# Kernel optimization log

Measured on AMD Instinct MI355X. Metric: run time of the kernel, lower is better.

Reference implementation:

```python
import jax, jax.numpy as jnp
import numpy as np

B, D, NH, HH, WW = 16, 384, 12, 48, 48
MLP = 4 * D


def _dwconv(x_blc, w, b, H, W):
    # depthwise 3x3 conv on (B,L,C) token map laid out as HxW
    Bsz, L, C = x_blc.shape
    xn = x_blc.reshape(Bsz, H, W, C).transpose(0, 3, 1, 2)  # NCHW
    y = jax.lax.conv_general_dilated(
        xn, w, (1, 1), 'SAME', feature_group_count=C,
        dimension_numbers=('NCHW', 'OIHW', 'NCHW'))
    y = y + b[None, :, None, None]
    return y.transpose(0, 2, 3, 1).reshape(Bsz, L, C)


def _ln(x, w, b):
    m = jnp.mean(x, -1, keepdims=True)
    v = jnp.mean(jnp.square(x - m), -1, keepdims=True)
    return (x - m) * jax.lax.rsqrt(v + 1e-5) * w + b


def _rope_tables(H, W, C):
    k_max = C // 4  # feature_dim // (2 * len((h, w)))
    theta = 1.0 / (10000.0 ** (jnp.arange(k_max, dtype=jnp.float32) / k_max))
    ah = jnp.broadcast_to((jnp.arange(H, dtype=jnp.float32)[:, None] * theta)[:, None, :], (H, W, k_max))
    aw = jnp.broadcast_to((jnp.arange(W, dtype=jnp.float32)[:, None] * theta)[None, :, :], (H, W, k_max))
    ang = jnp.concatenate([ah, aw], -1)  # (H, W, C//2)
    return jnp.cos(ang), jnp.sin(ang)


def _rope(x, cos, sin):
    # x: (B,H,W,C); complex rotation on consecutive pairs of the last dim
    xr = x.reshape(*x.shape[:-1], -1, 2)
    a, b2 = xr[..., 0], xr[..., 1]
    out = jnp.stack([cos * a - sin * b2, sin * a + cos * b2], -1)
    return out.reshape(x.shape)


def _forward(x, H, W, cpe1_w, cpe1_b, norm1_w, norm1_b, in_proj_w, in_proj_b,
             act_proj_w, act_proj_b, dwc_w, dwc_b, qk_w, qk_b, lepe_w, lepe_b,
             out_proj_w, out_proj_b, cpe2_w, cpe2_b, norm2_w, norm2_b,
             fc1_w, fc1_b, fc2_w, fc2_b):
    Bsz, L, C = x.shape
    nh = NH
    hd = C // nh

    x = x + _dwconv(x, cpe1_w, cpe1_b, H, W)
    shortcut = x
    xn = _ln(x, norm1_w, norm1_b)
    act_res = jax.nn.silu(xn @ act_proj_w.T + act_proj_b)
    xi = xn @ in_proj_w.T + in_proj_b
    xi = jax.nn.silu(_dwconv(xi, dwc_w, dwc_b, H, W))

    # --- linear (kernelized) attention with RoPE ---
    qk = xi @ qk_w.T + qk_b  # (B, L, 2C)
    q = jax.nn.elu(qk[..., :C]) + 1.0
    k = jax.nn.elu(qk[..., C:]) + 1.0
    cos, sin = _rope_tables(H, W, C)
    q_rope = _rope(q.reshape(Bsz, H, W, C), cos, sin).reshape(Bsz, L, nh, hd).transpose(0, 2, 1, 3)
    k_rope = _rope(k.reshape(Bsz, H, W, C), cos, sin).reshape(Bsz, L, nh, hd).transpose(0, 2, 1, 3)
    qh = q.reshape(Bsz, L, nh, hd).transpose(0, 2, 1, 3)
    kh = k.reshape(Bsz, L, nh, hd).transpose(0, 2, 1, 3)
    vh = xi.reshape(Bsz, L, nh, hd).transpose(0, 2, 1, 3)

    z = 1.0 / (jnp.einsum('bhnd,bhd->bhn', qh, kh.mean(axis=2)) + 1e-6)  # (B,nh,L)
    kv = jnp.einsum('bhnd,bhne->bhde', k_rope, vh) / L                   # (B,nh,hd,hd)
    att = jnp.einsum('bhnd,bhde->bhne', q_rope, kv) * z[..., None]
    att = att.transpose(0, 2, 1, 3).reshape(Bsz, L, C)
    att = att + _dwconv(xi, lepe_w, lepe_b, H, W)  # lepe on v (== xi)

    out = (att * act_res) @ out_proj_w.T + out_proj_b
    x = shortcut + out
    x = x + _dwconv(x, cpe2_w, cpe2_b, H, W)
    xn2 = _ln(x, norm2_w, norm2_b)
    h1 = jax.nn.gelu(xn2 @ fc1_w.T + fc1_b, approximate=False)
    x = x + (h1 @ fc2_w.T + fc2_b)
    return x


def setup_inputs() -> dict:
    key = jax.random.key(0)
    ks = jax.random.split(key, 16)
    def w(k, shape, s=0.02):
        return jax.random.normal(k, shape, jnp.float32) * s
    return {
        'x': jax.random.normal(ks[0], (B, HH * WW, D), jnp.float32),
        'H': HH, 'W': WW,
        'cpe1_w': w(ks[1], (D, 1, 3, 3)), 'cpe1_b': jnp.zeros((D,), jnp.float32),
        'norm1_w': jnp.ones((D,), jnp.float32), 'norm1_b': jnp.zeros((D,), jnp.float32),
        'in_proj_w': w(ks[2], (D, D)), 'in_proj_b': jnp.zeros((D,), jnp.float32),
        'act_proj_w': w(ks[3], (D, D)), 'act_proj_b': jnp.zeros((D,), jnp.float32),
        'dwc_w': w(ks[4], (D, 1, 3, 3)), 'dwc_b': jnp.zeros((D,), jnp.float32),
        'qk_w': w(ks[5], (2 * D, D)), 'qk_b': jnp.zeros((2 * D,), jnp.float32),
        'lepe_w': w(ks[6], (D, 1, 3, 3)), 'lepe_b': jnp.zeros((D,), jnp.float32),
        'out_proj_w': w(ks[7], (D, D)), 'out_proj_b': jnp.zeros((D,), jnp.float32),
        'cpe2_w': w(ks[8], (D, 1, 3, 3)), 'cpe2_b': jnp.zeros((D,), jnp.float32),
        'norm2_w': jnp.ones((D,), jnp.float32), 'norm2_b': jnp.zeros((D,), jnp.float32),
        'fc1_w': w(ks[9], (MLP, D)), 'fc1_b': jnp.zeros((MLP,), jnp.float32),
        'fc2_w': w(ks[10], (D, MLP)), 'fc2_b': jnp.zeros((D,), jnp.float32),
    }


def reference(x, H, W, cpe1_w, cpe1_b, norm1_w, norm1_b, in_proj_w, in_proj_b,
              act_proj_w, act_proj_b, dwc_w, dwc_b, qk_w, qk_b, lepe_w, lepe_b,
              out_proj_w, out_proj_b, cpe2_w, cpe2_b, norm2_w, norm2_b,
              fc1_w, fc1_b, fc2_w, fc2_b):
    return _forward(x, H, W, cpe1_w, cpe1_b, norm1_w, norm1_b, in_proj_w, in_proj_b,
                    act_proj_w, act_proj_b, dwc_w, dwc_b, qk_w, qk_b, lepe_w, lepe_b,
                    out_proj_w, out_proj_b, cpe2_w, cpe2_b, norm2_w, norm2_b,
                    fc1_w, fc1_b, fc2_w, fc2_b)
```

## Files before the change

### kernel.cpp

```cpp
#include <hip/hip_runtime.h>
#include <hip/hip_bf16.h>
#include <math.h>


#define L_TOK 2304
#define DIM   384
#define NHEADS 12
#define BATCH 16
#define HIMG  48
#define WIMG  48
#define UNITB ((size_t)L_TOK * DIM)

typedef unsigned short u16;
typedef __attribute__((ext_vector_type(8))) short bf16x8;
typedef __attribute__((ext_vector_type(8))) unsigned short u16x8;
typedef __attribute__((ext_vector_type(4))) float f32x4;

enum { M_BIAS = 0, M_SILU = 1, M_ELU1 = 2, M_GELU = 3, M_RES = 4 };

__device__ __forceinline__ float siluf(float x) { return x / (1.0f + __expf(-x)); }
__device__ __forceinline__ float geluf(float x) {
    float t = x * fmaf(x * x, 0.0713548162726f, 1.59576912161f);
    return x / (1.0f + __expf(-t));
}
__device__ __forceinline__ u16 f2bf(float f) {
    union { __hip_bfloat16 h; u16 u; } c;
    c.h = __float2bfloat16(f);
    return c.u;
}
__device__ __forceinline__ float bf2f(u16 u) { return __uint_as_float(((unsigned)u) << 16); }
__device__ __forceinline__ float4 bf2f4(ushort4 v) {
    return (float4){bf2f(v.x), bf2f(v.y), bf2f(v.z), bf2f(v.w)};
}
__device__ __forceinline__ void vmwait(int n) {
    if (n == 0)       asm volatile("s_waitcnt vmcnt(0)" ::: "memory");
    else if (n == 4)  asm volatile("s_waitcnt vmcnt(4)" ::: "memory");
    else if (n == 8)  asm volatile("s_waitcnt vmcnt(8)" ::: "memory");
    else if (n == 12) asm volatile("s_waitcnt vmcnt(12)" ::: "memory");
    else              asm volatile("s_waitcnt vmcnt(0)" ::: "memory");
}

__global__ void sentinel_k(float* out, float v) { out[0] = v; }

__global__ __launch_bounds__(256) void cvtw_k(const float* __restrict__ src, u16* __restrict__ dst) {
    int i = blockIdx.x * 256 + threadIdx.x;
    float4 v = ((const float4*)src)[i];
    ushort4 o;
    o.x = f2bf(v.x); o.y = f2bf(v.y); o.z = f2bf(v.z); o.w = f2bf(v.w);
    ((ushort4*)dst)[i] = o;
}

__global__ __launch_bounds__(256) void rope_tab_k(float* __restrict__ cosT, float* __restrict__ sinT) {
    int i = blockIdx.x * 256 + threadIdx.x;
    if (i >= L_TOK * 192) return;
    int n = i / 192, p = i % 192;
    int h = n / WIMG, w = n % WIMG;
    int j = (p < 96) ? p : p - 96;
    float pos = (p < 96) ? (float)h : (float)w;
    float theta = expf(-(float)j * (9.210340371976184f / 96.0f));
    float ang = pos * theta;
    cosT[i] = cosf(ang);
    sinT[i] = sinf(ang);
}

#define FMA4(s, a, ww) { s.x = fmaf(a.x, ww.x, s.x); s.y = fmaf(a.y, ww.y, s.y); \
                         s.z = fmaf(a.z, ww.z, s.z); s.w = fmaf(a.w, ww.w, s.w); }

__global__ __launch_bounds__(256) void dwconvf_k(const float* __restrict__ src,
                                                 const float* __restrict__ wgt,
                                                 const float* __restrict__ bias,
                                                 float* __restrict__ outf) {
    const int col = blockIdx.x * 256 + threadIdx.x;
    const int strip = blockIdx.y & 3;
    const int b = blockIdx.y >> 2;
    const int cg = col % 96, w = col / 96;
    const int rs = WIMG * DIM;
    const size_t ibase = (size_t)b * UNITB + (size_t)w * DIM + cg * 4;
    const float* srcb = src + ibase;
    const float4 z4 = {0.f, 0.f, 0.f, 0.f};
    float4 w9[9];
#pragma unroll
    for (int t = 0; t < 9; ++t) {
        const int c = cg * 4;
        w9[t] = (float4){wgt[(c + 0) * 9 + t], wgt[(c + 1) * 9 + t],
                         wgt[(c + 2) * 9 + t], wgt[(c + 3) * 9 + t]};
    }
    const float4 bv = ((const float4*)bias)[cg];
    float4 A0, A1, A2, B0, B1, B2, C0, C1, C2;
    auto ldrow = [&](int hh, float4& L0, float4& L1, float4& L2) {
        if ((unsigned)hh >= (unsigned)HIMG) { L0 = z4; L1 = z4; L2 = z4; return; }
        const float* p = srcb + (size_t)hh * rs;
        L0 = (w > 0)        ? *(const float4*)(p - DIM) : z4;
        L1 = *(const float4*)p;
        L2 = (w < WIMG - 1) ? *(const float4*)(p + DIM) : z4;
    };
    const int h0 = strip * 12;
    ldrow(h0 - 1, A0, A1, A2);
    ldrow(h0,     B0, B1, B2);
    for (int h = h0; h < h0 + 12; ++h) {
        ldrow(h + 1, C0, C1, C2);
        float4 s = bv;
        FMA4(s, A0, w9[0]); FMA4(s, A1, w9[1]); FMA4(s, A2, w9[2]);
        FMA4(s, B0, w9[3]); FMA4(s, B1, w9[4]); FMA4(s, B2, w9[5]);
        FMA4(s, C0, w9[6]); FMA4(s, C1, w9[7]); FMA4(s, C2, w9[8]);
        const size_t idx = ibase + (size_t)h * rs;
        s.x += B1.x; s.y += B1.y; s.z += B1.z; s.w += B1.w;
        *(float4*)(outf + idx) = s;
        A0 = B0; A1 = B1; A2 = B2;
        B0 = C0; B1 = C1; B2 = C2;
    }
}

__global__ __launch_bounds__(256) void dwconvb_k(const u16* __restrict__ src,
                                                 const float* __restrict__ wgt,
                                                 const float* __restrict__ bias,
                                                 const u16* __restrict__ att,
                                                 const u16* __restrict__ act,
                                                 u16* __restrict__ outb, int mode) {
    const int col = blockIdx.x * 256 + threadIdx.x;
    const int strip = blockIdx.y & 3;
    const int b = blockIdx.y >> 2;
    const int cg = col % 96, w = col / 96;
    const int rs = WIMG * DIM;
    const size_t ibase = (size_t)b * UNITB + (size_t)w * DIM + cg * 4;
    const u16* srcb = src + ibase;
    const float4 z4 = {0.f, 0.f, 0.f, 0.f};
    float4 w9[9];
#pragma unroll
    for (int t = 0; t < 9; ++t) {
        const int c = cg * 4;
        w9[t] = (float4){wgt[(c + 0) * 9 + t], wgt[(c + 1) * 9 + t],
                         wgt[(c + 2) * 9 + t], wgt[(c + 3) * 9 + t]};
    }
    const float4 bv = ((const float4*)bias)[cg];
    float4 A0, A1, A2, B0, B1, B2, C0, C1, C2;
    auto ldrow = [&](int hh, float4& L0, float4& L1, float4& L2) {
        if ((unsigned)hh >= (unsigned)HIMG) { L0 = z4; L1 = z4; L2 = z4; return; }
        const u16* p = srcb + (size_t)hh * rs;
        L0 = (w > 0)        ? bf2f4(*(const ushort4*)(p - DIM)) : z4;
        L1 = bf2f4(*(const ushort4*)p);
        L2 = (w < WIMG - 1) ? bf2f4(*(const ushort4*)(p + DIM)) : z4;
    };
    const int h0 = strip * 12;
    ldrow(h0 - 1, A0, A1, A2);
    ldrow(h0,     B0, B1, B2);
    for (int h = h0; h < h0 + 12; ++h) {
        ldrow(h + 1, C0, C1, C2);
        float4 s = bv;
        FMA4(s, A0, w9[0]); FMA4(s, A1, w9[1]); FMA4(s, A2, w9[2]);
        FMA4(s, B0, w9[3]); FMA4(s, B1, w9[4]); FMA4(s, B2, w9[5]);
        FMA4(s, C0, w9[6]); FMA4(s, C1, w9[7]); FMA4(s, C2, w9[8]);
        const size_t idx = ibase + (size_t)h * rs;
        ushort4 ob;
        if (mode == 1) {
            ob = (ushort4){f2bf(siluf(s.x)), f2bf(siluf(s.y)), f2bf(siluf(s.z)), f2bf(siluf(s.w))};
        } else {
            float4 a4 = bf2f4(*(const ushort4*)(att + idx));
            float4 m4 = bf2f4(*(const ushort4*)(act + idx));
            ob = (ushort4){f2bf((a4.x + s.x) * m4.x), f2bf((a4.y + s.y) * m4.y),
                           f2bf((a4.z + s.z) * m4.z), f2bf((a4.w + s.w) * m4.w)};
        }
        *(ushort4*)(outb + idx) = ob;
        A0 = B0; A1 = B1; A2 = B2;
        B0 = C0; B1 = C1; B2 = C2;
    }
}

__global__ __launch_bounds__(256) void ln_k(const float* __restrict__ in,
                                            const float* __restrict__ w,
                                            const float* __restrict__ b,
                                            u16* __restrict__ out) {
    const int row = blockIdx.x * 4 + (threadIdx.x >> 6);
    const int lane = threadIdx.x & 63;
    const float* x = in + (size_t)row * DIM;
    float v[6];
    float s = 0.f;
#pragma unroll
    for (int i = 0; i < 6; ++i) { v[i] = x[lane + i * 64]; s += v[i]; }
#pragma unroll
    for (int o = 32; o > 0; o >>= 1) s += __shfl_xor(s, o, 64);
    const float mean = s * (1.0f / DIM);
    float q = 0.f;
#pragma unroll
    for (int i = 0; i < 6; ++i) { float d = v[i] - mean; q = fmaf(d, d, q); }
#pragma unroll
    for (int o = 32; o > 0; o >>= 1) q += __shfl_xor(q, o, 64);
    const float rs = 1.0f / sqrtf(q * (1.0f / DIM) + 1e-5f);
    u16* o2 = out + (size_t)row * DIM;
#pragma unroll
    for (int i = 0; i < 6; ++i) {
        int d = lane + i * 64;
        o2[d] = f2bf(fmaf((v[i] - mean) * rs, w[d], b[d]));
    }
}

#define CHK 64
template<int K>
__global__ __launch_bounds__(256, 4) void gemm_sk(const u16* __restrict__ A, int lda,
                                                  const u16* __restrict__ Wt, int ldw,
                                                  const float* __restrict__ bias,
                                                  const float* __restrict__ bias2,
                                                  const float* __restrict__ res,
                                                  float* __restrict__ Cf, u16* __restrict__ Cb,
                                                  u16* __restrict__ Cb2,
                                                  int ldc, int mode, int mode2) {
    constexpr int NT = K / 32;
    constexpr int NCH = K / CHK;
    __shared__ u16 smem[16384];
    u16* const Bbuf[2] = {smem, smem + 8192};
    const int tid = threadIdx.x;
    const int l = tid & 63;
    const int w = tid >> 6;
    const int fr = l & 15, kb = l >> 4;
    const int T = gridDim.x * gridDim.y;
    const int d = blockIdx.y * gridDim.x + blockIdx.x;
    int flat = d;
    if ((T & 7) == 0) { const int q8 = T >> 3; flat = (d & 7) * q8 + (d >> 3); }
    const int n0 = (flat % gridDim.x) * 128;
    const int m0 = (flat / gridDim.x) * 128;
    const int sw = (fr & 7) << 4;

    f32x4 acc[2][8];
#pragma unroll
    for (int i = 0; i < 2; ++i)
#pragma unroll
        for (int j = 0; j < 8; ++j) acc[i][j] = (f32x4){0.f, 0.f, 0.f, 0.f};

    const u16* Ar0 = A + (size_t)(m0 + w * 32 + fr) * lda + kb * 8;
    const u16* Ar1 = Ar0 + (size_t)16 * lda;

    auto STAGE = [&](u16* buf, int cc) {
        const int ck0 = cc * CHK;
#pragma unroll
        for (int q = 0; q < 4; ++q) {
            const int c16 = q * 256 + tid;
            const int col = c16 >> 3;
            const int kb16 = c16 & 7;
            const int koff = ((kb16 * 16) ^ ((col & 7) << 4)) >> 1;
            const u16* g = Wt + (size_t)(n0 + col) * ldw + ck0 + koff;
            __builtin_amdgcn_global_load_lds(
                (const __attribute__((address_space(1))) void*)g,
                (__attribute__((address_space(3))) void*)(buf + (size_t)(q * 256 + w * 64) * 8),
                16, 0, 0);
        }
    };

    bf16x8 pA[4][2];
    STAGE(Bbuf[0], 0);
    __builtin_amdgcn_sched_barrier(0);
#pragma unroll
    for (int i = 0; i < 4; ++i) {
        pA[i][0] = *(const bf16x8*)(Ar0 + i * 32);
        pA[i][1] = *(const bf16x8*)(Ar1 + i * 32);
    }
    __builtin_amdgcn_sched_barrier(0);
    STAGE(Bbuf[1], 1);
    __builtin_amdgcn_sched_barrier(0);
    vmwait(12);
    __builtin_amdgcn_s_barrier();

#pragma unroll
    for (int c = 0; c < NCH; ++c) {
        const u16* bp = Bbuf[c & 1];
#pragma unroll
        for (int ks = 0; ks < 2; ++ks) {
            const int t = 2 * c + ks;
            bf16x8 a0 = pA[t & 3][0], a1 = pA[t & 3][1];
            if (t + 4 < NT) {
                pA[t & 3][0] = *(const bf16x8*)(Ar0 + (t + 4) * 32);
                pA[t & 3][1] = *(const bf16x8*)(Ar1 + (t + 4) * 32);
            }
            const int kpart = (ks * 64 + kb * 16) ^ sw;
            const char* bsb = (const char*)bp + fr * 128 + kpart;
#pragma unroll
            for (int ni = 0; ni < 8; ++ni) {
                bf16x8 bfrag = *(const bf16x8*)(bsb + ni * (16 * 128));
                acc[0][ni] = __builtin_amdgcn_mfma_f32_16x16x32_bf16(a0, bfrag, acc[0][ni], 0, 0, 0);
                acc[1][ni] = __builtin_amdgcn_mfma_f32_16x16x32_bf16(a1, bfrag, acc[1][ni], 0, 0, 0);
            }
        }
        __builtin_amdgcn_sched_barrier(0);
        __builtin_amdgcn_s_barrier();
        __builtin_amdgcn_sched_barrier(0);
        if (c + 2 < NCH) STAGE(Bbuf[c & 1], c + 2);
        __builtin_amdgcn_sched_barrier(0);
        if (c + 1 < NCH)
            vmwait((c < NCH - 2) ? 8 : 0);
    }

    const int orow = (l >> 4) * 4, ocol = l & 15;
    if (Cb != nullptr) {
        const bool is2 = (Cb2 != nullptr) && (n0 >= DIM);
        u16* dst = is2 ? Cb2 : Cb;
        const int ldcs = is2 ? DIM : ldc;
        const int nc0 = is2 ? (n0 - DIM) : n0;
        const float* bp2 = is2 ? bias2 : bias;
        const int md = is2 ? mode2 : mode;
#pragma unroll
        for (int mi = 0; mi < 2; ++mi)
#pragma unroll
            for (int ni = 0; ni < 8; ++ni) {
                const int colL = ni * 16 + ocol;
                const float bv = bp2[nc0 + colL];
#pragma unroll
                for (int r = 0; r < 4; ++r) {
                    const int rowL = w * 32 + mi * 16 + orow + r;
                    float v = acc[mi][ni][r] + bv;
                    if (md == M_SILU)      v = siluf(v);
                    else if (md == M_ELU1) v = (v > 0.f) ? (v + 1.f) : __expf(v);
                    else if (md == M_GELU) v = geluf(v);
                    smem[rowL * 128 + (colL ^ ((rowL & 7) << 3))] = f2bf(v);
                }
            }
        __builtin_amdgcn_s_barrier();
        const int rr = tid >> 4, cc = tid & 15;
#pragma unroll
        for (int it = 0; it < 8; ++it) {
            const int row = it * 16 + rr;
            u16x8 v = *(const u16x8*)&smem[row * 128 + ((cc * 8) ^ ((row & 7) << 3))];
            *(u16x8*)(dst + (size_t)(m0 + row) * ldcs + nc0 + cc * 8) = v;
        }
    } else {
        float* smf = (float*)smem;
#pragma unroll
        for (int p = 0; p < 2; ++p) {
            if (p) __builtin_amdgcn_s_barrier();
#pragma unroll
            for (int mi = 0; mi < 2; ++mi)
#pragma unroll
                for (int ni = 0; ni < 4; ++ni) {
                    const int colL = ni * 16 + ocol;
                    const float bv = bias[n0 + p * 64 + colL];
#pragma unroll
                    for (int r = 0; r < 4; ++r) {
                        const int rowL = w * 32 + mi * 16 + orow + r;
                        float v = acc[mi][p * 4 + ni][r] + bv;
                        if (mode == M_SILU)      v = siluf(v);
                        else if (mode == M_ELU1) v = (v > 0.f) ? (v + 1.f) : __expf(v);
                        else if (mode == M_GELU) v = geluf(v);
                        smf[rowL * 64 + (colL ^ ((rowL & 3) << 4))] = v;
                    }
                }
            __builtin_amdgcn_s_barrier();
            const int rr = tid >> 4, cc = tid & 15;
#pragma unroll
            for (int it = 0; it < 8; ++it) {
                const int row = it * 16 + rr;
                float4 v = *(const float4*)&smf[row * 64 + ((cc * 4) ^ ((row & 3) << 4))];
                const size_t oi = (size_t)(m0 + row) * ldc + n0 + p * 64 + cc * 4;
                if (res) {
                    float4 rv = *(const float4*)(res + oi);
                    v.x += rv.x; v.y += rv.y; v.z += rv.z; v.w += rv.w;
                }
                *(float4*)(Cf + oi) = v;
            }
        }
    }
}

__global__ __launch_bounds__(384) void kmean_part_k(const u16* __restrict__ kbuf, float* __restrict__ part, int nb) {
    const int b = blockIdx.x, chunk = blockIdx.y;
    const int c = threadIdx.x;
    const u16* p = kbuf + ((size_t)(b * L_TOK + chunk * 256)) * DIM + c;
    float s = 0.f;
    for (int n = 0; n < 256; ++n) s += bf2f(p[(size_t)n * DIM]);
    part[(size_t)(chunk * nb + b) * DIM + c] = s;
}

__global__ __launch_bounds__(384) void kmean_fin_k(const float* __restrict__ part, float* __restrict__ km, int nb) {
    const int b = blockIdx.x, c = threadIdx.x;
    float s = 0.f;
#pragma unroll
    for (int ch = 0; ch < 9; ++ch) s += part[(size_t)(ch * nb + b) * DIM + c];
    km[b * DIM + c] = s * (1.0f / L_TOK);
}

__global__ __launch_bounds__(256) void kv_part_k(const u16* __restrict__ kbuf, const u16* __restrict__ xi,
                                                 const float* __restrict__ cosT, const float* __restrict__ sinT,
                                                 float* __restrict__ part) {
    const int bh = blockIdx.x >> 2, chunk = blockIdx.x & 3;
    const int b = bh / NHEADS, h = bh % NHEADS;
    __shared__ float ks[64][33];
    __shared__ float vs[64][33];
    const int tid = threadIdx.x;
    const int e0 = (tid & 15) * 2;
    const int d0 = (tid >> 4) * 2;
    float acc00 = 0.f, acc01 = 0.f, acc10 = 0.f, acc11 = 0.f;
    const int nbeg = chunk * 576, nend = nbeg + 576;
    for (int n0 = nbeg; n0 < nend; n0 += 64) {
#pragma unroll
        for (int j = 0; j < 4; ++j) {
            int pi = tid + j * 256;
            int tn = pi >> 4;
            int pd = pi & 15;
            int n = n0 + tn;
            unsigned kk = *(const unsigned*)(kbuf + ((size_t)(b * L_TOK + n)) * DIM + h * 32 + pd * 2);
            float ka = bf2f((u16)(kk & 0xffffu)), kb2 = bf2f((u16)(kk >> 16));
            float cs = cosT[n * 192 + h * 16 + pd];
            float sn = sinT[n * 192 + h * 16 + pd];
            ks[tn][pd * 2]     = cs * ka - sn * kb2;
            ks[tn][pd * 2 + 1] = sn * ka + cs * kb2;
        }
#pragma unroll
        for (int j = 0; j < 4; ++j) {
            int pi = tid + j * 256;
            int tn = pi >> 4;
            int dd = (pi & 15) * 2;
            unsigned vv = *(const unsigned*)(xi + ((size_t)(b * L_TOK + n0 + tn)) * DIM + h * 32 + dd);
            vs[tn][dd]     = bf2f((u16)(vv & 0xffffu));
            vs[tn][dd + 1] = bf2f((u16)(vv >> 16));
        }
        __syncthreads();
#pragma unroll 8
        for (int n = 0; n < 64; ++n) {
            float k0v = ks[n][d0], k1v = ks[n][d0 + 1];
            float v0 = vs[n][e0], v1 = vs[n][e0 + 1];
            acc00 = fmaf(k0v, v0, acc00);
            acc01 = fmaf(k0v, v1, acc01);
            acc10 = fmaf(k1v, v0, acc10);
            acc11 = fmaf(k1v, v1, acc11);
        }
        __syncthreads();
    }
    float* o = part + ((size_t)blockIdx.x * 32 + d0) * 32 + e0;
    o[0] = acc00; o[1] = acc01;
    o[32] = acc10; o[33] = acc11;
}

__global__ __launch_bounds__(256) void kv_fin_k(const float* __restrict__ part, float* __restrict__ kv) {
    const int bh = blockIdx.x;
    const int tid = threadIdx.x;
#pragma unroll
    for (int i = tid; i < 1024; i += 256) {
        float s = 0.f;
#pragma unroll
        for (int c = 0; c < 4; ++c) s += part[((size_t)(bh * 4 + c)) * 1024 + i];
        kv[(size_t)bh * 1024 + i] = s * (1.0f / L_TOK);
    }
}

__global__ __launch_bounds__(384) void att_k(const u16* __restrict__ q, const float* __restrict__ kv,
                                             const float* __restrict__ km,
                                             const float* __restrict__ cosT, const float* __restrict__ sinT,
                                             u16* __restrict__ out) {
    __shared__ float kvs[NHEADS * 32 * 32];
    __shared__ float kms[DIM];
    __shared__ float sq[DIM];
    __shared__ float sqr[DIM];
    const int b = blockIdx.x / 48;
    const int chunk = blockIdx.x % 48;
    const int tid = threadIdx.x;
    for (int i = tid; i < NHEADS * 1024; i += 384) kvs[i] = kv[(size_t)b * (NHEADS * 1024) + i];
    kms[tid] = km[b * DIM + tid];
    __syncthreads();
    const int h = tid >> 5, e = tid & 31;
    const int p = tid >> 1;
    const float* kvh = &kvs[h * 1024];
    for (int ni = 0; ni < 48; ++ni) {
        const int n = chunk * 48 + ni;
        const float qv = bf2f(q[((size_t)(b * L_TOK + n)) * DIM + tid]);
        sq[tid] = qv;
        __syncthreads();
        float a = sq[tid & ~1], bb = sq[tid | 1];
        float cs = cosT[n * 192 + p], sn = sinT[n * 192 + p];
        sqr[tid] = (tid & 1) ? fmaf(sn, a, cs * bb) : fmaf(cs, a, -sn * bb);
        float zp = qv * kms[tid];
#pragma unroll
        for (int o = 16; o > 0; o >>= 1) zp += __shfl_xor(zp, o, 32);
        const float z = 1.0f / (zp + 1e-6f);
        __syncthreads();
        float dot = 0.f;
        const float* qrh = &sqr[h * 32];
#pragma unroll 8
        for (int dd = 0; dd < 32; ++dd) dot = fmaf(qrh[dd], kvh[dd * 32 + e], dot);
        out[((size_t)(b * L_TOK + n)) * DIM + tid] = f2bf(z * dot);
        __syncthreads();
    }
}

extern "C" void kernel_launch(void* const* d_in, const int* in_sizes, int n_in,
                              void* d_out, int out_size, void* d_ws, size_t ws_size,
                              hipStream_t stream) {
    const float* x       = (const float*)d_in[0];
    const float* cpe1_w  = (const float*)d_in[3];
    const float* cpe1_b  = (const float*)d_in[4];
    const float* norm1_w = (const float*)d_in[5];
    const float* norm1_b = (const float*)d_in[6];
    const float* in_w    = (const float*)d_in[7];
    const float* in_b    = (const float*)d_in[8];
    const float* act_w   = (const float*)d_in[9];
    const float* act_b   = (const float*)d_in[10];
    const float* dwc_w   = (const float*)d_in[11];
    const float* dwc_b   = (const float*)d_in[12];
    const float* qk_w    = (const float*)d_in[13];
    const float* qk_b    = (const float*)d_in[14];
    const float* lepe_w  = (const float*)d_in[15];
    const float* lepe_b  = (const float*)d_in[16];
    const float* outp_w  = (const float*)d_in[17];
    const float* outp_b  = (const float*)d_in[18];
    const float* cpe2_w  = (const float*)d_in[19];
    const float* cpe2_b  = (const float*)d_in[20];
    const float* norm2_w = (const float*)d_in[21];
    const float* norm2_b = (const float*)d_in[22];
    const float* fc1_w   = (const float*)d_in[23];
    const float* fc1_b   = (const float*)d_in[24];
    const float* fc2_w   = (const float*)d_in[25];
    const float* fc2_b   = (const float*)d_in[26];
    float* out = (float*)d_out;

    float* ws = (float*)d_ws;
    const size_t TAB = (size_t)L_TOK * 192;
    const size_t NW_IN = 147456, NW_QK = 294912, NW_FC = 589824;
    const size_t WBF_U16 = NW_IN * 3 + NW_QK + NW_FC * 2;
    const size_t KVP = 4 * (size_t)BATCH * NHEADS * 1024;
    const size_t SMALL = 2 * TAB + (size_t)BATCH * DIM + 9 * (size_t)BATCH * DIM
                       + (size_t)BATCH * NHEADS * 1024 + KVP + WBF_U16 / 2;
    float* cosT = ws;
    float* sinT = cosT + TAB;
    float* km   = sinT + TAB;
    float* part = km + (size_t)BATCH * DIM;
    float* kvb  = part + 9 * (size_t)BATCH * DIM;
    float* kvp  = kvb + (size_t)BATCH * NHEADS * 1024;
    u16*   wb_in  = (u16*)(kvp + KVP);
    u16*   wb_act = wb_in + NW_IN;
    u16*   wb_qk  = wb_act + NW_IN;
    u16*   wb_out = wb_qk + NW_QK;
    u16*   wb_fc1 = wb_out + NW_IN;
    u16*   wb_fc2 = wb_fc1 + NW_FC;
    float* gbuf = ws + SMALL;

    const size_t avail = (ws_size / 4 > SMALL) ? (ws_size / 4 - SMALL) : 0;
    int nb = 0;
    for (int cand = BATCH; cand >= 1; cand >>= 1)
        if (9 * (size_t)cand * UNITB / 2 <= avail) { nb = cand; break; }
    if (nb == 0) {
        sentinel_k<<<1, 1, 0, stream>>>(out, (float)(ws_size >> 20));
        return;
    }

    cvtw_k<<<(int)(NW_IN / 1024), 256, 0, stream>>>(in_w, wb_in);
    cvtw_k<<<(int)(NW_IN / 1024), 256, 0, stream>>>(act_w, wb_act);
    cvtw_k<<<(int)(NW_QK / 1024), 256, 0, stream>>>(qk_w, wb_qk);
    cvtw_k<<<(int)(NW_IN / 1024), 256, 0, stream>>>(outp_w, wb_out);
    cvtw_k<<<(int)(NW_FC / 1024), 256, 0, stream>>>(fc1_w, wb_fc1);
    cvtw_k<<<(int)(NW_FC / 1024), 256, 0, stream>>>(fc2_w, wb_fc2);
    rope_tab_k<<<(int)((TAB + 255) / 256), 256, 0, stream>>>(cosT, sinT);

    for (int b0 = 0; b0 < BATCH; b0 += nb) {
        const size_t goff = (size_t)b0 * UNITB;
        const size_t GU   = (size_t)nb * UNITB;
        float* W0 = gbuf;
        float* W1 = gbuf + GU;
        float* W2 = gbuf + 2 * GU;
        u16*   Wb = (u16*)(gbuf + 4 * GU);
        float* O  = out + goff;
        const float* Xg = x + goff;
        u16* xi0p = (u16*)W2;
        u16* actp = (u16*)W2 + GU;

        const dim3 DWG(18, nb * 4);
        const dim3 G384(3, nb * 18), G768(6, nb * 18), G1536(12, nb * 18);

        dwconvf_k<<<DWG, 256, 0, stream>>>(Xg, cpe1_w, cpe1_b, W0);
        ln_k<<<nb * 576, 256, 0, stream>>>(W0, norm1_w, norm1_b, (u16*)W1);
        gemm_sk<384><<<G768, 256, 0, stream>>>((u16*)W1, DIM, wb_in, DIM, in_b, act_b, nullptr,
                                               nullptr, xi0p, actp, DIM, M_BIAS, M_SILU);
        dwconvb_k<<<DWG, 256, 0, stream>>>(xi0p, dwc_w, dwc_b, nullptr, nullptr, Wb, 1);
        gemm_sk<384><<<G768, 256, 0, stream>>>(Wb, DIM, wb_qk, DIM, qk_b, qk_b + DIM, nullptr,
                                               nullptr, (u16*)W1, (u16*)O, DIM, M_ELU1, M_ELU1);
        kmean_part_k<<<dim3(nb, 9), 384, 0, stream>>>((u16*)O, part, nb);
        kmean_fin_k<<<nb, 384, 0, stream>>>(part, km, nb);
        kv_part_k<<<nb * NHEADS * 4, 256, 0, stream>>>((u16*)O, Wb, cosT, sinT, kvp);
        kv_fin_k<<<nb * NHEADS, 256, 0, stream>>>(kvp, kvb);
        att_k<<<nb * 48, 384, 0, stream>>>((u16*)W1, kvb, km, cosT, sinT, (u16*)O);
        dwconvb_k<<<DWG, 256, 0, stream>>>(Wb, lepe_w, lepe_b, (const u16*)O, actp,
                                           (u16*)W1, 3);
        gemm_sk<384><<<G384, 256, 0, stream>>>((u16*)W1, DIM, wb_out, DIM, outp_b, nullptr, W0,
                                               W2, nullptr, nullptr, DIM, M_RES, M_RES);
        dwconvf_k<<<DWG, 256, 0, stream>>>(W2, cpe2_w, cpe2_b, W0);
        ln_k<<<nb * 576, 256, 0, stream>>>(W0, norm2_w, norm2_b, (u16*)W1);
        gemm_sk<384><<<G1536, 256, 0, stream>>>((u16*)W1, DIM, wb_fc1, DIM, fc1_b, nullptr, nullptr,
                                                nullptr, (u16*)W2, nullptr, 1536, M_GELU, M_GELU);
        gemm_sk<1536><<<G384, 256, 0, stream>>>((u16*)W2, 1536, wb_fc2, 1536, fc2_b, nullptr, W0,
                                                O, nullptr, nullptr, DIM, M_RES, M_RES);
    }
}
```

Before: 611.9 us.

## Replace scalar attention apply kernel with MFMA tile kernel plus separate normalizer pass

The per-token scalar attention kernel, which used shared-memory dot products and three barriers per token, is replaced by an MFMA-based kernel. It computes RoPE(q)·kv per (batch, head, 128-row tile) using bf16 16x16x32 MFMA, with kv transposed and stored as bf16. The normalizer z = 1/(q·kmean) moves into a separate small kernel that writes a per-row buffer. This trades a per-token serialized loop for matrix-core throughput, at the cost of an extra launch, an extra buffer, and bf16 rounding of kv and rotated q.

After: 530.5 us. 1.15x faster.

```diff
diff --git a/kernel.cpp b/kernel.cpp
--- a/kernel.cpp
+++ b/kernel.cpp
@@ -375,6 +375,21 @@
     km[b * DIM + c] = s * (1.0f / L_TOK);
 }
 
+__global__ __launch_bounds__(256) void z_k(const u16* __restrict__ q, const float* __restrict__ km,
+                                           float* __restrict__ z) {
+    const int row = blockIdx.x * 4 + (threadIdx.x >> 6);
+    const int lane = threadIdx.x & 63;
+    const int b = row / L_TOK;
+    const u16* qr = q + (size_t)row * DIM;
+    const float* kb = km + b * DIM;
+    float s = 0.f;
+#pragma unroll
+    for (int i = 0; i < 6; ++i) { int c = lane + i * 64; s += bf2f(qr[c]) * kb[c]; }
+#pragma unroll
+    for (int o = 32; o > 0; o >>= 1) s += __shfl_xor(s, o, 64);
+    if (lane == 0) z[row] = 1.0f / (s + 1e-6f);
+}
+
 __global__ __launch_bounds__(256) void kv_part_k(const u16* __restrict__ kbuf, const u16* __restrict__ xi,
                                                  const float* __restrict__ cosT, const float* __restrict__ sinT,
                                                  float* __restrict__ part) {
@@ -427,54 +442,89 @@
     o[32] = acc10; o[33] = acc11;
 }
 
-__global__ __launch_bounds__(256) void kv_fin_k(const float* __restrict__ part, float* __restrict__ kv) {
+__global__ __launch_bounds__(256) void kv_fin_k(const float* __restrict__ part, u16* __restrict__ kvt) {
     const int bh = blockIdx.x;
     const int tid = threadIdx.x;
 #pragma unroll
     for (int i = tid; i < 1024; i += 256) {
+        const int e = i >> 5, dd = i & 31;
         float s = 0.f;
 #pragma unroll
-        for (int c = 0; c < 4; ++c) s += part[((size_t)(bh * 4 + c)) * 1024 + i];
-        kv[(size_t)bh * 1024 + i] = s * (1.0f / L_TOK);
-    }
-}
-
-__global__ __launch_bounds__(384) void att_k(const u16* __restrict__ q, const float* __restrict__ kv,
-                                             const float* __restrict__ km,
-                                             const float* __restrict__ cosT, const float* __restrict__ sinT,
-                                             u16* __restrict__ out) {
-    __shared__ float kvs[NHEADS * 32 * 32];
-    __shared__ float kms[DIM];
-    __shared__ float sq[DIM];
-    __shared__ float sqr[DIM];
-    const int b = blockIdx.x / 48;
-    const int chunk = blockIdx.x % 48;
-    const int tid = threadIdx.x;
-    for (int i = tid; i < NHEADS * 1024; i += 384) kvs[i] = kv[(size_t)b * (NHEADS * 1024) + i];
-    kms[tid] = km[b * DIM + tid];
+        for (int c = 0; c < 4; ++c) s += part[((size_t)(bh * 4 + c)) * 1024 + dd * 32 + e];
+        kvt[(size_t)bh * 1024 + i] = f2bf(s * (1.0f / L_TOK));
+    }
+}
+
+__global__ __launch_bounds__(256) void attm_k(const u16* __restrict__ q, const u16* __restrict__ kvt,
+                                              const float* __restrict__ z,
+                                              const float* __restrict__ cosT, const float* __restrict__ sinT,
+                                              u16* __restrict__ out) {
+    __shared__ u16 ost[128 * 32];
+    const int tid = threadIdx.x, l = tid & 63, w = tid >> 6;
+    const int b = blockIdx.y / NHEADS, h = blockIdx.y % NHEADS;
+    const int m0 = blockIdx.x * 128;
+    const int fr = l & 15, kb = l >> 4;
+
+    f32x4 acc[2][2];
+#pragma unroll
+    for (int i = 0; i < 2; ++i)
+#pragma unroll
+        for (int j = 0; j < 2; ++j) acc[i][j] = (f32x4){0.f, 0.f, 0.f, 0.f};
+
+    const int p0 = h * 16 + kb * 4;
+    bf16x8 afr[2];
+#pragma unroll
+    for (int mi = 0; mi < 2; ++mi) {
+        const int n = m0 + w * 32 + mi * 16 + fr;
+        bf16x8 raw = *(const bf16x8*)(q + ((size_t)(b * L_TOK + n)) * DIM + h * 32 + kb * 8);
+        float4 cs = *(const float4*)(cosT + (size_t)n * 192 + p0);
+        float4 sn = *(const float4*)(sinT + (size_t)n * 192 + p0);
+        union { u16 u[8]; bf16x8 v; } pk;
+        float a0, a1;
+        a0 = bf2f((u16)raw[0]); a1 = bf2f((u16)raw[1]);
+        pk.u[0] = f2bf(cs.x * a0 - sn.x * a1); pk.u[1] = f2bf(sn.x * a0 + cs.x * a1);
+        a0 = bf2f((u16)raw[2]); a1 = bf2f((u16)raw[3]);
+        pk.u[2] = f2bf(cs.y * a0 - sn.y * a1); pk.u[3] = f2bf(sn.y * a0 + cs.y * a1);
+        a0 = bf2f((u16)raw[4]); a1 = bf2f((u16)raw[5]);
+        pk.u[4] = f2bf(cs.z * a0 - sn.z * a1); pk.u[5] = f2bf(sn.z * a0 + cs.z * a1);
+        a0 = bf2f((u16)raw[6]); a1 = bf2f((u16)raw[7]);
+        pk.u[6] = f2bf(cs.w * a0 - sn.w * a1); pk.u[7] = f2bf(sn.w * a0 + cs.w * a1);
+        afr[mi] = pk.v;
+    }
+    bf16x8 bfr[2];
+    const u16* kvh = kvt + (size_t)(b * NHEADS + h) * 1024;
+#pragma unroll
+    for (int ni = 0; ni < 2; ++ni)
+        bfr[ni] = *(const bf16x8*)(kvh + (ni * 16 + fr) * 32 + kb * 8);
+#pragma unroll
+    for (int mi = 0; mi < 2; ++mi)
+#pragma unroll
+        for (int ni = 0; ni < 2; ++ni)
+            acc[mi][ni] = __builtin_amdgcn_mfma_f32_16x16x32_bf16(afr[mi], bfr[ni], acc[mi][ni], 0, 0, 0);
+
+    const int orow = (l >> 4) * 4, ocol = l & 15;
+#pragma unroll
+    for (int mi = 0; mi < 2; ++mi) {
+        float zz[4];
+#pragma unroll
+        for (int r = 0; r < 4; ++r)
+            zz[r] = z[b * L_TOK + m0 + w * 32 + mi * 16 + orow + r];
+#pragma unroll
+        for (int ni = 0; ni < 2; ++ni) {
+#pragma unroll
+            for (int r = 0; r < 4; ++r) {
+                const int rowL = w * 32 + mi * 16 + orow + r;
+                ost[rowL * 32 + ni * 16 + ocol] = f2bf(acc[mi][ni][r] * zz[r]);
+            }
+        }
+    }
     __syncthreads();
-    const int h = tid >> 5, e = tid & 31;
-    const int p = tid >> 1;
-    const float* kvh = &kvs[h * 1024];
-    for (int ni = 0; ni < 48; ++ni) {
-        const int n = chunk * 48 + ni;
-        const float qv = bf2f(q[((size_t)(b * L_TOK + n)) * DIM + tid]);
-        sq[tid] = qv;
-        __syncthreads();
-        float a = sq[tid & ~1], bb = sq[tid | 1];
-        float cs = cosT[n * 192 + p], sn = sinT[n * 192 + p];
-        sqr[tid] = (tid & 1) ? fmaf(sn, a, cs * bb) : fmaf(cs, a, -sn * bb);
-        float zp = qv * kms[tid];
-#pragma unroll
-        for (int o = 16; o > 0; o >>= 1) zp += __shfl_xor(zp, o, 32);
-        const float z = 1.0f / (zp + 1e-6f);
-        __syncthreads();
-        float dot = 0.f;
-        const float* qrh = &sqr[h * 32];
-#pragma unroll 8
-        for (int dd = 0; dd < 32; ++dd) dot = fmaf(qrh[dd], kvh[dd * 32 + e], dot);
-        out[((size_t)(b * L_TOK + n)) * DIM + tid] = f2bf(z * dot);
-        __syncthreads();
+#pragma unroll
+    for (int it = 0; it < 2; ++it) {
+        const int ch = it * 256 + tid;
+        const int row = ch >> 2, c8 = (ch & 3) * 8;
+        u16x8 v = *(const u16x8*)&ost[row * 32 + c8];
+        *(u16x8*)(out + ((size_t)(b * L_TOK + m0 + row)) * DIM + h * 32 + c8) = v;
     }
 }
 
@@ -513,15 +563,18 @@
     const size_t NW_IN = 147456, NW_QK = 294912, NW_FC = 589824;
     const size_t WBF_U16 = NW_IN * 3 + NW_QK + NW_FC * 2;
     const size_t KVP = 4 * (size_t)BATCH * NHEADS * 1024;
+    const size_t ZB  = (size_t)BATCH * L_TOK;
     const size_t SMALL = 2 * TAB + (size_t)BATCH * DIM + 9 * (size_t)BATCH * DIM
-                       + (size_t)BATCH * NHEADS * 1024 + KVP + WBF_U16 / 2;
+                       + (size_t)BATCH * NHEADS * 1024 + KVP + ZB + WBF_U16 / 2;
     float* cosT = ws;
     float* sinT = cosT + TAB;
     float* km   = sinT + TAB;
     float* part = km + (size_t)BATCH * DIM;
     float* kvb  = part + 9 * (size_t)BATCH * DIM;
     float* kvp  = kvb + (size_t)BATCH * NHEADS * 1024;
-    u16*   wb_in  = (u16*)(kvp + KVP);
+    float* zb   = kvp + KVP;
+    u16*   kvt  = (u16*)kvb;
+    u16*   wb_in  = (u16*)(zb + ZB);
     u16*   wb_act = wb_in + NW_IN;
     u16*   wb_qk  = wb_act + NW_IN;
     u16*   wb_out = wb_qk + NW_QK;
@@ -570,9 +623,10 @@
                                                nullptr, (u16*)W1, (u16*)O, DIM, M_ELU1, M_ELU1);
         kmean_part_k<<<dim3(nb, 9), 384, 0, stream>>>((u16*)O, part, nb);
         kmean_fin_k<<<nb, 384, 0, stream>>>(part, km, nb);
+        z_k<<<nb * 576, 256, 0, stream>>>((u16*)W1, km, zb);
         kv_part_k<<<nb * NHEADS * 4, 256, 0, stream>>>((u16*)O, Wb, cosT, sinT, kvp);
-        kv_fin_k<<<nb * NHEADS, 256, 0, stream>>>(kvp, kvb);
-        att_k<<<nb * 48, 384, 0, stream>>>((u16*)W1, kvb, km, cosT, sinT, (u16*)O);
+        kv_fin_k<<<nb * NHEADS, 256, 0, stream>>>(kvp, kvt);
+        attm_k<<<dim3(18, nb * NHEADS), 256, 0, stream>>>((u16*)W1, kvt, zb, cosT, sinT, (u16*)O);
         dwconvb_k<<<DWG, 256, 0, stream>>>(Wb, lepe_w, lepe_b, (const u16*)O, actp,
                                            (u16*)W1, 3);
         gemm_sk<384><<<G384, 256, 0, stream>>>((u16*)W1, DIM, wb_out, DIM, outp_b, nullptr, W0,
```
